# Optimization experiments

Hardware: AMD Instinct MI355X
Metric: run time of the kernel (lower is better)

Reference implementation:

```python
import jax, jax.numpy as jnp
import numpy as np

B, T, C = 8, 2048, 1024
CONTEXT_SIZE = T  # repo ties context_size to sequence length of the mask


def setup_inputs() -> dict:
    key = jax.random.key(0)
    ks = jax.random.split(key, 7)
    s = 1.0 / np.sqrt(C)
    return {
        "x": jax.random.normal(ks[0], (B, T, C), dtype=jnp.float32),
        "Wq": jax.random.normal(ks[1], (C, C), dtype=jnp.float32) * s,
        "bq": jax.random.normal(ks[2], (C,), dtype=jnp.float32) * s,
        "Wk": jax.random.normal(ks[3], (C, C), dtype=jnp.float32) * s,
        "bk": jax.random.normal(ks[4], (C,), dtype=jnp.float32) * s,
        "Wv": jax.random.normal(ks[5], (C, C), dtype=jnp.float32) * s,
        "bv": jax.random.normal(ks[6], (C,), dtype=jnp.float32) * s,
    }


def reference(x, Wq, bq, Wk, bk, Wv, bv):
    # x: [B, T, C]; weights stored as [in, out] so y = x @ W + b (same math as nn.Linear)
    Tlen = x.shape[1]
    q = x @ Wq + bq
    k = x @ Wk + bk
    v = x @ Wv + bv
    # NOTE: original scales by context_size**-0.5 (seq-length based), not head-dim
    scale = jnp.asarray(CONTEXT_SIZE, x.dtype) ** -0.5
    scores = jnp.einsum("btc,bsc->bts", q, k) * scale  # [B, T, T]
    causal = jnp.tril(jnp.ones((Tlen, Tlen), dtype=bool))
    scores = jnp.where(causal, scores, -jnp.inf)
    attn = jax.nn.softmax(scores, axis=-1)
    return jnp.einsum("bts,bsc->btc", attn, v)
```

## Files before the change

kernel.cpp:

```cpp
#include <hip/hip_runtime.h>

#define B_SZ 8
#define T_SZ 2048
#define C_SZ 1024

typedef __attribute__((ext_vector_type(8))) short short8;
typedef __attribute__((ext_vector_type(8))) unsigned short ushort8;
typedef __attribute__((ext_vector_type(4))) float f32x4;

__device__ __forceinline__ unsigned short f2bf(float x) {
  union { float f; unsigned u; } v; v.f = x;
  unsigned r = v.u + 0x7FFFu + ((v.u >> 16) & 1u);
  return (unsigned short)(r >> 16);
}
__device__ __forceinline__ float bf2f(unsigned short h) {
  union { unsigned u; float f; } v; v.u = ((unsigned)h) << 16;
  return v.f;
}

__device__ __forceinline__ void gload16(const void* g, void* l) {
  __builtin_amdgcn_global_load_lds(
      (const __attribute__((address_space(1))) unsigned int*)(uintptr_t)g,
      (__attribute__((address_space(3))) unsigned int*)(uintptr_t)l, 16, 0, 0);
}

__device__ __forceinline__ int xcd_swz(int orig, int nwg) {
  return (orig & 7) * (nwg >> 3) + (orig >> 3);
}

#define WAITV(N) asm volatile("s_waitcnt vmcnt(" #N ")" ::: "memory")
#define BAR1                            \
  {                                     \
    asm volatile("" ::: "memory");      \
    __builtin_amdgcn_s_barrier();       \
    __builtin_amdgcn_sched_barrier(0);  \
    asm volatile("" ::: "memory");      \
  }
#define BAR2                            \
  {                                     \
    asm volatile("" ::: "memory");      \
    __builtin_amdgcn_s_barrier();       \
    asm volatile("" ::: "memory");      \
  }

template <int LDA, int LDB>
__device__ __forceinline__ void nt8p(const unsigned short* __restrict__ Ab,
                                     const unsigned short* __restrict__ Bb,
                                     const int NT, unsigned short* lds,
                                     f32x4 (&acc)[2][4][4]) {
  const int lane = threadIdx.x & 63;
  const int wid = threadIdx.x >> 6;
  const int wr = wid >> 2;
  const int wc = wid & 3;
  const int fr = lane & 15;
  const int fq = lane >> 4;

  const int aslot = ((lane & 7) ^ (lane >> 3)) * 8;
  const int rr0 = (wid * 2 + 0) * 8 + (lane >> 3);
  const int rr1 = (wid * 2 + 1) * 8 + (lane >> 3);
  const unsigned short* pA0 =
      Ab + (size_t)((rr0 >> 6) * 128 + (rr0 & 63)) * LDA + aslot;
  const unsigned short* pA1 =
      Ab + (size_t)((rr1 >> 6) * 128 + (rr1 & 63)) * LDA + aslot;
  const int bslot = ((lane & 3) ^ ((lane >> 3) & 3)) * 8;
  const unsigned short* pB0 =
      Bb + (size_t)((wid * 2 + 0) * 16 + (lane >> 2)) * LDB + bslot;
  const unsigned short* pB1 =
      Bb + (size_t)((wid * 2 + 1) * 16 + (lane >> 2)) * LDB + bslot;
  const int ldsC0 = (wid * 2 + 0) * 512;
  const int ldsC1 = (wid * 2 + 1) * 512;

  const int arb = wr * 4096 + fr * 64;
  const int asw0 = ((0 * 4 + fq) ^ (fr & 7)) * 8;
  const int asw1 = ((1 * 4 + fq) ^ (fr & 7)) * 8;
  const int brb =
      16384 + (wc * 64 + fr) * 32 + ((fq ^ ((fr >> 1) & 3)) * 8);

#define STG_A(d, h, kt)                                           \
  {                                                               \
    gload16(pA0 + (size_t)(h) * 64 * LDA + (size_t)(kt) * 64,     \
            lds + (d) * 32768 + (h) * 8192 + ldsC0);              \
    gload16(pA1 + (size_t)(h) * 64 * LDA + (size_t)(kt) * 64,     \
            lds + (d) * 32768 + (h) * 8192 + ldsC1);              \
  }
#define STG_B(d, kh, kt)                                          \
  {                                                               \
    gload16(pB0 + (kh) * 32 + (size_t)(kt) * 64,                  \
            lds + (d) * 32768 + 16384 + (kh) * 8192 + ldsC0);     \
    gload16(pB1 + (kh) * 32 + (size_t)(kt) * 64,                  \
            lds + (d) * 32768 + 16384 + (kh) * 8192 + ldsC1);     \
  }
#define LDAF(d, r, s)                                             \
  _Pragma("unroll") for (int mb = 0; mb < 4; ++mb) af[mb] =       \
      *(const short8*)&lds[(d) * 32768 + (r) * 8192 + arb +       \
                           mb * 1024 + ((s) ? asw1 : asw0)];
#define LDBF(d, s)                                                \
  _Pragma("unroll") for (int nb = 0; nb < 4; ++nb) bf[nb] =       \
      *(const short8*)&lds[(d) * 32768 + (s) * 8192 + brb + nb * 512];
#define MM(r)                                                     \
  __builtin_amdgcn_s_setprio(1);                                  \
  _Pragma("unroll") for (int mb = 0; mb < 4; ++mb)                \
  _Pragma("unroll") for (int nb = 0; nb < 4; ++nb)                \
  acc[r][mb][nb] = __builtin_amdgcn_mfma_f32_16x16x32_bf16(       \
      af[mb], bf[nb], acc[r][mb][nb], 0, 0, 0);                   \
  __builtin_amdgcn_s_setprio(0);
#define TILE_STEP(d, dn, TT)                                                 \
  {                                                                          \
    const int tp1 = ((TT) + 1 < NT) ? (TT) + 1 : NT - 1;                     \
    const int tp2 = ((TT) + 2 < NT) ? (TT) + 2 : NT - 1;                     \
    short8 af[4], bf[4];                                                     \
    LDAF(d, 0, 0); LDBF(d, 0); STG_B(dn, 1, tp1); BAR1; MM(0); WAITV(6); BAR2; \
    LDAF(d, 1, 0); STG_A(dn, 1, tp1); BAR1; MM(1); BAR2;                     \
    LDAF(d, 0, 1); LDBF(d, 1); STG_B(d, 0, tp2); BAR1; MM(0); BAR2;          \
    LDAF(d, 1, 1); STG_A(d, 0, tp2); BAR1; MM(1); WAITV(8); BAR2;            \
  }

  const int t1 = (NT > 1) ? 1 : 0;
  STG_B(0, 0, 0);
  STG_A(0, 0, 0);
  STG_B(0, 1, 0);
  STG_A(0, 1, 0);
  STG_B(1, 0, t1);
  STG_A(1, 0, t1);
  WAITV(8);
  BAR2;

  for (int T = 0; T < NT; T += 2) {
    TILE_STEP(0, 1, T);
    TILE_STEP(1, 0, T + 1);
  }
#undef STG_A
#undef STG_B
#undef LDAF
#undef LDBF
#undef MM
#undef TILE_STEP
}

__global__ __launch_bounds__(256) void convert_x(const float* __restrict__ x,
                                                 unsigned short* __restrict__ Xb,
                                                 int n8) {
  for (int i = blockIdx.x * blockDim.x + threadIdx.x; i < n8;
       i += gridDim.x * blockDim.x) {
    const float4* p = (const float4*)(x + (size_t)i * 8);
    float4 a = p[0], b = p[1];
    ushort8 u;
    u[0] = f2bf(a.x); u[1] = f2bf(a.y); u[2] = f2bf(a.z); u[3] = f2bf(a.w);
    u[4] = f2bf(b.x); u[5] = f2bf(b.y); u[6] = f2bf(b.z); u[7] = f2bf(b.w);
    *(ushort8*)(Xb + (size_t)i * 8) = u;
  }
}

__global__ __launch_bounds__(256) void transpose_w(
    const float* __restrict__ Wq, const float* __restrict__ Wk,
    const float* __restrict__ Wv, unsigned short* __restrict__ Wt) {
  const int z = blockIdx.z;
  const float* W = z == 0 ? Wq : (z == 1 ? Wk : Wv);
  unsigned short* O = Wt + (size_t)z * C_SZ * C_SZ;
  __shared__ float tl[32][33];
  const int bx = blockIdx.x * 32;
  const int by = blockIdx.y * 32;
  const int tx = threadIdx.x & 31;
  const int ty = threadIdx.x >> 5;
#pragma unroll
  for (int j = 0; j < 4; ++j)
    tl[ty + j * 8][tx] = W[(size_t)(by + ty + j * 8) * C_SZ + bx + tx];
  __syncthreads();
#pragma unroll
  for (int j = 0; j < 4; ++j)
    O[(size_t)(bx + ty + j * 8) * C_SZ + by + tx] = f2bf(tl[tx][ty + j * 8]);
}

__global__ __launch_bounds__(256) void transpose_v(
    const unsigned short* __restrict__ V, unsigned short* __restrict__ Vt) {
  const int b = blockIdx.z;
  __shared__ unsigned short tl[64][66];
  const int bx = blockIdx.x * 64;
  const int by = blockIdx.y * 64;
  const int tx = threadIdx.x & 63;
  const int ty = threadIdx.x >> 6;
  const unsigned short* Vb = V + (size_t)b * T_SZ * C_SZ;
  unsigned short* Ob = Vt + (size_t)b * C_SZ * T_SZ;
#pragma unroll
  for (int r = 0; r < 16; ++r)
    tl[ty * 16 + r][tx] = Vb[(size_t)(by + ty * 16 + r) * C_SZ + bx + tx];
  __syncthreads();
#pragma unroll
  for (int r = 0; r < 16; ++r)
    Ob[(size_t)(bx + ty * 16 + r) * T_SZ + by + tx] = tl[tx][ty * 16 + r];
}

__global__ __launch_bounds__(512, 1) void qkv_fused(
    const unsigned short* __restrict__ Xb, const unsigned short* __restrict__ Wt,
    const float* __restrict__ bq, const float* __restrict__ bk,
    const float* __restrict__ bv, unsigned short* __restrict__ QKV) {
  __shared__ unsigned short lds[65536] __attribute__((aligned(128)));
  const int wg = xcd_swz(blockIdx.x, 3 * 64 * 4);
  const int z = wg >> 8;
  const int rem = wg & 255;
  const int m0 = (rem >> 2) * 256;
  const int n0 = (rem & 3) * 256;
  const float* bias = z == 0 ? bq : (z == 1 ? bk : bv);

  f32x4 acc[2][4][4] = {};
  nt8p<C_SZ, C_SZ>(Xb + (size_t)m0 * C_SZ,
                   Wt + (size_t)z * C_SZ * C_SZ + (size_t)n0 * C_SZ,
                   C_SZ / 64, lds, acc);

  unsigned short* Y = QKV + (size_t)z * B_SZ * T_SZ * C_SZ;
  const int lane = threadIdx.x & 63;
  const int wid = threadIdx.x >> 6;
  const int wr = wid >> 2, wc = wid & 3;
  const int fr = lane & 15, fq = lane >> 4;
#pragma unroll
  for (int r = 0; r < 2; ++r)
#pragma unroll
    for (int nb = 0; nb < 4; ++nb) {
      const int col = n0 + wc * 64 + nb * 16 + fr;
      const float bvv = bias[col];
#pragma unroll
      for (int mb = 0; mb < 4; ++mb) {
        const int row0 = m0 + wr * 128 + r * 64 + mb * 16 + fq * 4;
#pragma unroll
        for (int j = 0; j < 4; ++j)
          Y[(size_t)(row0 + j) * C_SZ + col] = f2bf(acc[r][mb][nb][j] + bvv);
      }
    }
}

__global__ __launch_bounds__(512, 1) void scores_gemm(
    const unsigned short* __restrict__ Q, const unsigned short* __restrict__ Km,
    unsigned short* __restrict__ S, float scale) {
  const int wg = xcd_swz(blockIdx.x, B_SZ * 8 * 8);
  const int b = wg >> 6;
  const int rem = wg & 63;
  const int mt = rem >> 3, nt = rem & 7;
  if (nt > mt) return;
  const int m0 = mt * 256, n0 = nt * 256;
  __shared__ unsigned short lds[65536] __attribute__((aligned(128)));

  f32x4 acc[2][4][4] = {};
  nt8p<C_SZ, C_SZ>(Q + (size_t)b * T_SZ * C_SZ + (size_t)m0 * C_SZ,
                   Km + (size_t)b * T_SZ * C_SZ + (size_t)n0 * C_SZ,
                   C_SZ / 64, lds, acc);

  unsigned short* Sb = S + (size_t)b * T_SZ * T_SZ;
  const int lane = threadIdx.x & 63;
  const int wid = threadIdx.x >> 6;
  const int wr = wid >> 2, wc = wid & 3;
  const int fr = lane & 15, fq = lane >> 4;
#pragma unroll
  for (int r = 0; r < 2; ++r)
#pragma unroll
    for (int nb = 0; nb < 4; ++nb) {
      const int col = n0 + wc * 64 + nb * 16 + fr;
#pragma unroll
      for (int mb = 0; mb < 4; ++mb) {
        const int row0 = m0 + wr * 128 + r * 64 + mb * 16 + fq * 4;
#pragma unroll
        for (int j = 0; j < 4; ++j)
          Sb[(size_t)(row0 + j) * T_SZ + col] = f2bf(acc[r][mb][nb][j] * scale);
      }
    }
}

__device__ __forceinline__ float wredmax(float v) {
#pragma unroll
  for (int o = 32; o > 0; o >>= 1) v = fmaxf(v, __shfl_xor(v, o, 64));
  return v;
}
__device__ __forceinline__ float wredsum(float v) {
#pragma unroll
  for (int o = 32; o > 0; o >>= 1) v += __shfl_xor(v, o, 64);
  return v;
}

__global__ __launch_bounds__(256) void softmax_causal(
    unsigned short* __restrict__ S) {
  const int row = blockIdx.x;
  const int b = row >> 11;
  const int tq = row & (T_SZ - 1);
  unsigned short* sr = S + (size_t)b * T_SZ * T_SZ + (size_t)tq * T_SZ;
  const int len = tq + 1;
  const int wlen = (len + 255) & ~255;
  const int tid = threadIdx.x;
  const int lane = tid & 63;
  const int wid = tid >> 6;
  const int i0 = tid * 8;
  __shared__ float red[4];

  const ushort8 raw = *(const ushort8*)(sr + i0);
  float v[8];
  float mx = -1e30f;
#pragma unroll
  for (int j = 0; j < 8; ++j) {
    v[j] = (i0 + j < len) ? bf2f(raw[j]) : -1e30f;
    mx = fmaxf(mx, v[j]);
  }
  mx = wredmax(mx);
  if (lane == 0) red[wid] = mx;
  __syncthreads();
  mx = fmaxf(fmaxf(red[0], red[1]), fmaxf(red[2], red[3]));
  __syncthreads();

  float sm = 0.f;
#pragma unroll
  for (int j = 0; j < 8; ++j) {
    v[j] = __expf(v[j] - mx);
    sm += v[j];
  }
  sm = wredsum(sm);
  if (lane == 0) red[wid] = sm;
  __syncthreads();
  sm = red[0] + red[1] + red[2] + red[3];
  const float inv = 1.f / sm;

  if (i0 < wlen) {
    ushort8 o;
#pragma unroll
    for (int j = 0; j < 8; ++j)
      o[j] = (i0 + j < len) ? f2bf(v[j] * inv) : (unsigned short)0;
    *(ushort8*)(sr + i0) = o;
  }
}

__global__ __launch_bounds__(512, 1) void pv_gemm(
    const unsigned short* __restrict__ P, const unsigned short* __restrict__ Vt,
    float* __restrict__ O) {
  const int wg = xcd_swz(blockIdx.x, B_SZ * 8 * 4);
  const int b = wg >> 5;
  const int rem = wg & 31;
  const int mt = rem >> 2, nt = rem & 3;
  const int m0 = mt * 256, n0 = nt * 256;
  __shared__ unsigned short lds[65536] __attribute__((aligned(128)));

  f32x4 acc[2][4][4] = {};
  nt8p<T_SZ, T_SZ>(P + (size_t)b * T_SZ * T_SZ + (size_t)m0 * T_SZ,
                   Vt + (size_t)b * C_SZ * T_SZ + (size_t)n0 * T_SZ,
                   4 * (mt + 1), lds, acc);

  float* Ob = O + (size_t)b * T_SZ * C_SZ;
  const int lane = threadIdx.x & 63;
  const int wid = threadIdx.x >> 6;
  const int wr = wid >> 2, wc = wid & 3;
  const int fr = lane & 15, fq = lane >> 4;
#pragma unroll
  for (int r = 0; r < 2; ++r)
#pragma unroll
    for (int nb = 0; nb < 4; ++nb) {
      const int col = n0 + wc * 64 + nb * 16 + fr;
#pragma unroll
      for (int mb = 0; mb < 4; ++mb) {
        const int row0 = m0 + wr * 128 + r * 64 + mb * 16 + fq * 4;
#pragma unroll
        for (int j = 0; j < 4; ++j)
          Ob[(size_t)(row0 + j) * C_SZ + col] = acc[r][mb][nb][j];
      }
    }
}

extern "C" void kernel_launch(void* const* d_in, const int* in_sizes, int n_in,
                              void* d_out, int out_size, void* d_ws,
                              size_t ws_size, hipStream_t stream) {
  (void)in_sizes; (void)n_in; (void)out_size; (void)ws_size;
  const float* x = (const float*)d_in[0];
  const float* Wq = (const float*)d_in[1];
  const float* bq = (const float*)d_in[2];
  const float* Wk = (const float*)d_in[3];
  const float* bk = (const float*)d_in[4];
  const float* Wv = (const float*)d_in[5];
  const float* bv = (const float*)d_in[6];
  float* out = (float*)d_out;

  const size_t TC = (size_t)B_SZ * T_SZ * C_SZ;
  unsigned short* Q = (unsigned short*)d_ws;
  unsigned short* K = Q + TC;
  unsigned short* V = K + TC;
  unsigned short* S = V + TC;
  unsigned short* Xb = S;
  unsigned short* Wt = S + TC;
  unsigned short* Vt = Q;

  const float scale = 0.022097086912079608f;

  hipLaunchKernelGGL(convert_x, dim3(2048), dim3(256), 0, stream, x, Xb,
                     (int)(TC / 8));
  hipLaunchKernelGGL(transpose_w, dim3(32, 32, 3), dim3(256), 0, stream, Wq,
                     Wk, Wv, Wt);
  hipLaunchKernelGGL(qkv_fused, dim3(3 * 64 * 4), dim3(512), 0, stream, Xb, Wt,
                     bq, bk, bv, Q);
  hipLaunchKernelGGL(scores_gemm, dim3(B_SZ * 8 * 8), dim3(512), 0, stream, Q,
                     K, S, scale);
  hipLaunchKernelGGL(transpose_v, dim3(16, 32, 8), dim3(256), 0, stream, V,
                     Vt);
  hipLaunchKernelGGL(softmax_causal, dim3(B_SZ * T_SZ), dim3(256), 0, stream,
                     S);
  hipLaunchKernelGGL(pv_gemm, dim3(B_SZ * 8 * 4), dim3(512), 0, stream, S, Vt,
                     out);
}
```

Measured before the change: 268.8 us.

## Fuse V transpose into QKV epilogue and raise GEMM occupancy to two blocks

The QKV GEMM epilogue now writes V directly in transposed layout: each wave stages its accumulators in LDS and emits contiguous bf16 vectors along T. This removes the separate transpose_v kernel and its full read and write of V. The three GEMMs also change launch bounds from (512,1) to (512,2), which caps registers per thread to allow two resident blocks, and they add an explicit wait before the epilogue. Softmax rows skip the global load for lanes past the causal length. The 128 KB static LDS per block may still limit residency to one block, and the tighter register cap risks spills.

```diff
diff --git a/kernel.cpp b/kernel.cpp
--- a/kernel.cpp
+++ b/kernel.cpp
@@ -73,8 +73,7 @@
   const int arb = wr * 4096 + fr * 64;
   const int asw0 = ((0 * 4 + fq) ^ (fr & 7)) * 8;
   const int asw1 = ((1 * 4 + fq) ^ (fr & 7)) * 8;
-  const int brb =
-      16384 + (wc * 64 + fr) * 32 + ((fq ^ ((fr >> 1) & 3)) * 8);
+  const int brb = 16384 + (wc * 64 + fr) * 32 + ((fq ^ ((fr >> 1) & 3)) * 8);
 
 #define STG_A(d, h, kt)                                           \
   {                                                               \
@@ -137,6 +136,13 @@
 #undef TILE_STEP
 }
 
+#define EPI_DUMP(r, mh)                                               \
+  _Pragma("unroll") for (int mb2 = 0; mb2 < 2; ++mb2)                 \
+  _Pragma("unroll") for (int nb = 0; nb < 4; ++nb)                    \
+  _Pragma("unroll") for (int j = 0; j < 4; ++j)                       \
+      ldw[(mb2 * 16 + fq * 4 + j) * 66 + nb * 16 + fr] =              \
+          acc[r][(mh) * 2 + mb2][nb][j];
+
 __global__ __launch_bounds__(256) void convert_x(const float* __restrict__ x,
                                                  unsigned short* __restrict__ Xb,
                                                  int n8) {
@@ -171,64 +177,76 @@
     O[(size_t)(bx + ty + j * 8) * C_SZ + by + tx] = f2bf(tl[tx][ty + j * 8]);
 }
 
-__global__ __launch_bounds__(256) void transpose_v(
-    const unsigned short* __restrict__ V, unsigned short* __restrict__ Vt) {
-  const int b = blockIdx.z;
-  __shared__ unsigned short tl[64][66];
-  const int bx = blockIdx.x * 64;
-  const int by = blockIdx.y * 64;
-  const int tx = threadIdx.x & 63;
-  const int ty = threadIdx.x >> 6;
-  const unsigned short* Vb = V + (size_t)b * T_SZ * C_SZ;
-  unsigned short* Ob = Vt + (size_t)b * C_SZ * T_SZ;
-#pragma unroll
-  for (int r = 0; r < 16; ++r)
-    tl[ty * 16 + r][tx] = Vb[(size_t)(by + ty * 16 + r) * C_SZ + bx + tx];
-  __syncthreads();
-#pragma unroll
-  for (int r = 0; r < 16; ++r)
-    Ob[(size_t)(bx + ty * 16 + r) * T_SZ + by + tx] = tl[tx][ty * 16 + r];
-}
-
-__global__ __launch_bounds__(512, 1) void qkv_fused(
+__global__ __launch_bounds__(512, 2) void qkv_fused(
     const unsigned short* __restrict__ Xb, const unsigned short* __restrict__ Wt,
     const float* __restrict__ bq, const float* __restrict__ bk,
-    const float* __restrict__ bv, unsigned short* __restrict__ QKV) {
+    const float* __restrict__ bv, unsigned short* __restrict__ Q,
+    unsigned short* __restrict__ K, unsigned short* __restrict__ Vt) {
   __shared__ unsigned short lds[65536] __attribute__((aligned(128)));
   const int wg = xcd_swz(blockIdx.x, 3 * 64 * 4);
   const int z = wg >> 8;
   const int rem = wg & 255;
   const int m0 = (rem >> 2) * 256;
   const int n0 = (rem & 3) * 256;
-  const float* bias = z == 0 ? bq : (z == 1 ? bk : bv);
 
   f32x4 acc[2][4][4] = {};
   nt8p<C_SZ, C_SZ>(Xb + (size_t)m0 * C_SZ,
                    Wt + (size_t)z * C_SZ * C_SZ + (size_t)n0 * C_SZ,
                    C_SZ / 64, lds, acc);
-
-  unsigned short* Y = QKV + (size_t)z * B_SZ * T_SZ * C_SZ;
+  WAITV(0);
+
   const int lane = threadIdx.x & 63;
   const int wid = threadIdx.x >> 6;
   const int wr = wid >> 2, wc = wid & 3;
   const int fr = lane & 15, fq = lane >> 4;
-#pragma unroll
-  for (int r = 0; r < 2; ++r)
-#pragma unroll
-    for (int nb = 0; nb < 4; ++nb) {
-      const int col = n0 + wc * 64 + nb * 16 + fr;
-      const float bvv = bias[col];
-#pragma unroll
-      for (int mb = 0; mb < 4; ++mb) {
-        const int row0 = m0 + wr * 128 + r * 64 + mb * 16 + fq * 4;
-#pragma unroll
-        for (int j = 0; j < 4; ++j)
-          Y[(size_t)(row0 + j) * C_SZ + col] = f2bf(acc[r][mb][nb][j] + bvv);
+
+  if (z < 2) {
+    unsigned short* Y = (z == 0) ? Q : K;
+    const float* bias = (z == 0) ? bq : bk;
+#pragma unroll
+    for (int r = 0; r < 2; ++r)
+#pragma unroll
+      for (int nb = 0; nb < 4; ++nb) {
+        const int col = n0 + wc * 64 + nb * 16 + fr;
+        const float bvv = bias[col];
+#pragma unroll
+        for (int mb = 0; mb < 4; ++mb) {
+          const int row0 = m0 + wr * 128 + r * 64 + mb * 16 + fq * 4;
+#pragma unroll
+          for (int j = 0; j < 4; ++j)
+            Y[(size_t)(row0 + j) * C_SZ + col] = f2bf(acc[r][mb][nb][j] + bvv);
+        }
       }
-    }
-}
-
-__global__ __launch_bounds__(512, 1) void scores_gemm(
+  } else {
+    __syncthreads();
+    float* ldw = (float*)lds + wid * 2112;
+    const int b2 = m0 >> 11;
+    const int tb = m0 & (T_SZ - 1);
+    unsigned short* Vtb = Vt + (size_t)b2 * C_SZ * T_SZ;
+    const int cb = n0 + wc * 64;
+    float bv4[4];
+#pragma unroll
+    for (int i = 0; i < 4; ++i) bv4[i] = bv[cb + (lane >> 2) + i * 16];
+#pragma unroll
+    for (int r = 0; r < 2; ++r)
+#pragma unroll
+      for (int mh = 0; mh < 2; ++mh) {
+        EPI_DUMP(r, mh);
+        const int t0 = tb + wr * 128 + r * 64 + mh * 32 + (lane & 3) * 8;
+#pragma unroll
+        for (int i = 0; i < 4; ++i) {
+          const int c = (lane >> 2) + i * 16;
+          ushort8 o;
+#pragma unroll
+          for (int k = 0; k < 8; ++k)
+            o[k] = f2bf(ldw[((lane & 3) * 8 + k) * 66 + c] + bv4[i]);
+          *(ushort8*)&Vtb[(size_t)(cb + c) * T_SZ + t0] = o;
+        }
+      }
+  }
+}
+
+__global__ __launch_bounds__(512, 2) void scores_gemm(
     const unsigned short* __restrict__ Q, const unsigned short* __restrict__ Km,
     unsigned short* __restrict__ S, float scale) {
   const int wg = xcd_swz(blockIdx.x, B_SZ * 8 * 8);
@@ -243,6 +261,7 @@
   nt8p<C_SZ, C_SZ>(Q + (size_t)b * T_SZ * C_SZ + (size_t)m0 * C_SZ,
                    Km + (size_t)b * T_SZ * C_SZ + (size_t)n0 * C_SZ,
                    C_SZ / 64, lds, acc);
+  WAITV(0);
 
   unsigned short* Sb = S + (size_t)b * T_SZ * T_SZ;
   const int lane = threadIdx.x & 63;
@@ -289,13 +308,18 @@
   const int i0 = tid * 8;
   __shared__ float red[4];
 
-  const ushort8 raw = *(const ushort8*)(sr + i0);
   float v[8];
   float mx = -1e30f;
-#pragma unroll
-  for (int j = 0; j < 8; ++j) {
-    v[j] = (i0 + j < len) ? bf2f(raw[j]) : -1e30f;
-    mx = fmaxf(mx, v[j]);
+  if (i0 < len) {
+    const ushort8 raw = *(const ushort8*)(sr + i0);
+#pragma unroll
+    for (int j = 0; j < 8; ++j) {
+      v[j] = (i0 + j < len) ? bf2f(raw[j]) : -1e30f;
+      mx = fmaxf(mx, v[j]);
+    }
+  } else {
+#pragma unroll
+    for (int j = 0; j < 8; ++j) v[j] = -1e30f;
   }
   mx = wredmax(mx);
   if (lane == 0) red[wid] = mx;
@@ -324,7 +348,7 @@
   }
 }
 
-__global__ __launch_bounds__(512, 1) void pv_gemm(
+__global__ __launch_bounds__(512, 2) void pv_gemm(
     const unsigned short* __restrict__ P, const unsigned short* __restrict__ Vt,
     float* __restrict__ O) {
   const int wg = xcd_swz(blockIdx.x, B_SZ * 8 * 4);
@@ -338,6 +362,7 @@
   nt8p<T_SZ, T_SZ>(P + (size_t)b * T_SZ * T_SZ + (size_t)m0 * T_SZ,
                    Vt + (size_t)b * C_SZ * T_SZ + (size_t)n0 * T_SZ,
                    4 * (mt + 1), lds, acc);
+  WAITV(0);
 
   float* Ob = O + (size_t)b * T_SZ * C_SZ;
   const int lane = threadIdx.x & 63;
@@ -375,11 +400,10 @@
   const size_t TC = (size_t)B_SZ * T_SZ * C_SZ;
   unsigned short* Q = (unsigned short*)d_ws;
   unsigned short* K = Q + TC;
-  unsigned short* V = K + TC;
-  unsigned short* S = V + TC;
+  unsigned short* Vt = K + TC;
+  unsigned short* S = Vt + TC;
   unsigned short* Xb = S;
   unsigned short* Wt = S + TC;
-  unsigned short* Vt = Q;
 
   const float scale = 0.022097086912079608f;
 
@@ -388,11 +412,9 @@
   hipLaunchKernelGGL(transpose_w, dim3(32, 32, 3), dim3(256), 0, stream, Wq,
                      Wk, Wv, Wt);
   hipLaunchKernelGGL(qkv_fused, dim3(3 * 64 * 4), dim3(512), 0, stream, Xb, Wt,
-                     bq, bk, bv, Q);
+                     bq, bk, bv, Q, K, Vt);
   hipLaunchKernelGGL(scores_gemm, dim3(B_SZ * 8 * 8), dim3(512), 0, stream, Q,
                      K, S, scale);
-  hipLaunchKernelGGL(transpose_v, dim3(16, 32, 8), dim3(256), 0, stream, V,
-                     Vt);
   hipLaunchKernelGGL(softmax_causal, dim3(B_SZ * T_SZ), dim3(256), 0, stream,
                      S);
   hipLaunchKernelGGL(pv_gemm, dim3(B_SZ * 8 * 4), dim3(512), 0, stream, S, Vt,
```

Result: faster. 256.0 us, median of 2 (-4.8%).
